# Kernel tuning notes

Hardware: AMD Instinct MI355X
Metric: run time of the kernel (lower is better)

## Reference

```python
import jax, jax.numpy as jnp
import numpy as np

T, B, D, H = 512, 64, 1024, 1024

def setup_inputs() -> dict:
    key = jax.random.key(0)
    k1, k2, k3 = jax.random.split(key, 3)
    x = jax.random.normal(k1, (T, B, D), dtype=jnp.float32)
    c0 = jnp.zeros((B, H), dtype=jnp.float32)
    h0 = jnp.zeros((B, H), dtype=jnp.float32)
    # fused gate weights, gate order (i, f, g, o) as in flax LSTMCell
    Wi = jax.random.normal(k2, (D, 4 * H), dtype=jnp.float32) / np.float32(np.sqrt(D))
    Wh = jax.random.normal(k3, (H, 4 * H), dtype=jnp.float32) / np.float32(np.sqrt(H))
    b = jnp.zeros((4 * H,), dtype=jnp.float32)
    return {"x": x, "c0": c0, "h0": h0, "Wi": Wi, "Wh": Wh, "b": b}

def reference(x, c0, h0, Wi, Wh, b):
    # scanned LSTM: per step z = x_t @ Wi + h @ Wh + b -> gates i,f,g,o
    def step(carry, xt):
        c, h = carry
        z = xt @ Wi + h @ Wh + b  # [B, 4H]
        i, f, g, o = jnp.split(z, 4, axis=-1)
        i = jax.nn.sigmoid(i)
        f = jax.nn.sigmoid(f)
        g = jnp.tanh(g)
        o = jax.nn.sigmoid(o)
        c_new = f * c + i * g
        h_new = o * jnp.tanh(c_new)
        return (c_new, h_new), h_new

    (cT, hT), ys = jax.lax.scan(step, (c0, h0), x)
    return ys, cT, hT
```

## Files before the change

### kernel.cpp

```cpp
#include <hip/hip_runtime.h>
#include <hip/hip_bf16.h>
#include <stdint.h>

typedef __attribute__((ext_vector_type(8))) short bf16x8;
typedef __attribute__((ext_vector_type(4))) float floatx4;

#define TT 512
#define BB 64
#define DD 1024
#define HH 1024
#define YS_ELEMS 33554432UL

#define OFF_A     0UL
#define OFF_XB    268435456UL
#define OFF_WIT   335544320UL
#define OFF_WHT   343932928UL
#define OFF_HBUF  352321536UL
#define OFF_FLAGS 352583680UL

#define NBLK 64
#define WPITCH 2064
#define LDSW_BYTES (64 * WPITCH)
#define LDSR_FLOATS (2 * 64 * 33)
#define SMEM_BYTES (LDSW_BYTES + LDSR_FLOATS * 4)

__device__ __forceinline__ unsigned short f2bf(float f) {
  union { float f; unsigned u; } v; v.f = f;
  unsigned r = (v.u + 0x7fffu + ((v.u >> 16) & 1u)) >> 16;
  return (unsigned short)r;
}
__device__ __forceinline__ float bf2f(unsigned short s) {
  union { unsigned u; float f; } v; v.u = ((unsigned)s) << 16;
  return v.f;
}
__device__ __forceinline__ float sigm(float x) { return 1.0f / (1.0f + __expf(-x)); }
__device__ __forceinline__ float tanh_fast(float x) { return 1.0f - 2.0f / (1.0f + __expf(2.0f * x)); }
__device__ __forceinline__ float ap_get(uint2 p, int r) {
  unsigned u = (r < 2) ? p.x : p.y;
  return bf2f((unsigned short)(u >> ((r & 1) * 16)));
}
__device__ __forceinline__ void gload_lds16(const void* g, void* l) {
  __builtin_amdgcn_global_load_lds((const __attribute__((address_space(1))) void*)g,
                                   (__attribute__((address_space(3))) void*)l, 16, 0, 0);
}
__device__ __forceinline__ bf16x8 ldg_b128_if(const void* p) {
  bf16x8 v;
  asm volatile("global_load_dwordx4 %0, %1, off sc0 sc1"
               : "=v"(v) : "v"(p) : "memory");
  return v;
}
__device__ __forceinline__ int ldg_b32_if(const void* p) {
  int v;
  asm volatile("global_load_dword %0, %1, off sc0 sc1\n\ts_waitcnt vmcnt(0)"
               : "=v"(v) : "v"(p) : "memory");
  return v;
}
__device__ __forceinline__ void stg_b64_if(void* p, uint2 v) {
  asm volatile("global_store_dwordx2 %0, %1, off sc0 sc1"
               :: "v"(p), "v"(v) : "memory");
}
__device__ __forceinline__ void stg_b32_if(void* p, int v) {
  asm volatile("global_store_dword %0, %1, off sc0 sc1"
               :: "v"(p), "v"(v) : "memory");
}

__global__ void convert_kernel(const float* __restrict__ x, const float* __restrict__ h0,
                               unsigned short* __restrict__ xb, unsigned short* __restrict__ hb0) {
  const long total4 = (33554432L + 65536L) / 4;
  long stride = (long)gridDim.x * blockDim.x;
  for (long i = (long)blockIdx.x * blockDim.x + threadIdx.x; i < total4; i += stride) {
    long base = i * 4;
    const float4* src;
    unsigned short* dst;
    if (base < 33554432L) { src = (const float4*)(x + base); dst = xb + base; }
    else { src = (const float4*)(h0 + (base - 33554432L)); dst = hb0 + (base - 33554432L); }
    float4 v = *src;
    uint2 p;
    p.x = (unsigned)f2bf(v.x) | ((unsigned)f2bf(v.y) << 16);
    p.y = (unsigned)f2bf(v.z) | ((unsigned)f2bf(v.w) << 16);
    *(uint2*)dst = p;
  }
}

__global__ void transpose_kernel(const float* __restrict__ W, unsigned short* __restrict__ WT) {
  __shared__ float tile[32][33];
  int n0 = blockIdx.x * 32, k0 = blockIdx.y * 32;
  int tx = threadIdx.x & 31, ty = threadIdx.x >> 5;
#pragma unroll
  for (int r = 0; r < 4; r++)
    tile[ty + r * 8][tx] = W[(size_t)(k0 + ty + r * 8) * 4096 + n0 + tx];
  __syncthreads();
#pragma unroll
  for (int r = 0; r < 4; r++)
    WT[(size_t)(n0 + ty + r * 8) * 1024 + k0 + tx] = f2bf(tile[tx][ty + r * 8]);
}

__global__ __launch_bounds__(256) void gemm1_kernel(const unsigned short* __restrict__ xb,
                                                    const unsigned short* __restrict__ wiT,
                                                    const float* __restrict__ bias,
                                                    unsigned short* __restrict__ Aws) {
  __shared__ unsigned short ldsA[128 * 32];
  __shared__ unsigned short ldsB[128 * 32];
  int id = blockIdx.x;
  int xcd = id & 7, seq = id >> 3;
  int n0 = (xcd * 4 + (seq & 3)) * 128;
  int m0 = (seq >> 2) * 128;
  int tid = threadIdx.x, w = tid >> 6, l = tid & 63;
  int wm = w & 1, wn = w >> 1;
  int c = l & 15, q = l >> 4;
  const floatx4 fz = {0.f, 0.f, 0.f, 0.f};
  floatx4 acc[4][4];
#pragma unroll
  for (int mi = 0; mi < 4; mi++)
#pragma unroll
    for (int ni = 0; ni < 4; ni++) acc[mi][ni] = fz;

  const char* gA = (const char*)xb + (size_t)(m0 + w * 32 + (l >> 2)) * 2048 + (l & 3) * 16;
  const char* gB = (const char*)wiT + (size_t)(n0 + w * 32 + (l >> 2)) * 2048 + (l & 3) * 16;
  char* lA = (char*)ldsA + (w * 32) * 64;
  char* lB = (char*)ldsB + (w * 32) * 64;

  for (int kt = 0; kt < 32; kt++) {
    gload_lds16(gA, lA);
    gload_lds16(gA + 16 * 2048, lA + 16 * 64);
    gload_lds16(gB, lB);
    gload_lds16(gB + 16 * 2048, lB + 16 * 64);
    gA += 64; gB += 64;
    __syncthreads();
    bf16x8 a[4], b[4];
#pragma unroll
    for (int mi = 0; mi < 4; mi++)
      a[mi] = *(const bf16x8*)((const char*)ldsA + (wm * 64 + mi * 16 + c) * 64 + q * 16);
#pragma unroll
    for (int ni = 0; ni < 4; ni++)
      b[ni] = *(const bf16x8*)((const char*)ldsB + (wn * 64 + ni * 16 + c) * 64 + q * 16);
#pragma unroll
    for (int mi = 0; mi < 4; mi++)
#pragma unroll
      for (int ni = 0; ni < 4; ni++)
        acc[mi][ni] = __builtin_amdgcn_mfma_f32_16x16x32_bf16(a[mi], b[ni], acc[mi][ni], 0, 0, 0);
    __syncthreads();
  }
#pragma unroll
  for (int mi = 0; mi < 4; mi++) {
#pragma unroll
    for (int ni = 0; ni < 4; ni++) {
      int n_g = n0 + wn * 64 + ni * 16 + c;
      float bn = bias[n_g];
      size_t mbase = (size_t)m0 + wm * 64 + mi * 16 + q * 4;
      floatx4 v = acc[mi][ni];
      uint2 p;
      p.x = (unsigned)f2bf(v.x + bn) | ((unsigned)f2bf(v.y + bn) << 16);
      p.y = (unsigned)f2bf(v.z + bn) | ((unsigned)f2bf(v.w + bn) << 16);
      *(uint2*)((char*)Aws + (((size_t)n_g << 15) + mbase) * 2) = p;
    }
  }
}

__global__ __launch_bounds__(256, 1) void lstm_kernel(const unsigned short* __restrict__ Aws,
                                                      const unsigned short* __restrict__ whT,
                                                      const float* __restrict__ c0,
                                                      unsigned short* __restrict__ hbuf,
                                                      float* __restrict__ out,
                                                      int* __restrict__ flags) {
  extern __shared__ char smem[];
  char* ldsW = smem;
  float* ldsR = (float*)(smem + LDSW_BYTES);
  int tid = threadIdx.x, wid = tid >> 6, l = tid & 63;
  int wi = wid & 1, wj = wid >> 1;
  int c = l & 15, q = l >> 4;
  int hbase = blockIdx.x * 16;

  for (int i = tid; i < 64 * 128; i += 256) {
    int ln = i >> 7, ch = i & 127;
    int n_g = (ln >> 4) * 1024 + hbase + (ln & 15);
    *(uint4*)(ldsW + ln * WPITCH + ch * 16) =
        *(const uint4*)((const char*)whT + (size_t)n_g * 2048 + ch * 16);
  }
  float cst[2][4];
  if (wj == 0) {
#pragma unroll
    for (int mi = 0; mi < 2; mi++)
#pragma unroll
      for (int r = 0; r < 4; r++)
        cst[mi][r] = c0[(wi * 32 + mi * 16 + q * 4 + r) * 1024 + hbase + c];
  }
  __syncthreads();

  for (int t = 0; t < 512; t++) {
    uint2 ap[2][4];
    if (wj == 0) {
#pragma unroll
      for (int mi = 0; mi < 2; mi++)
#pragma unroll
        for (int nj = 0; nj < 4; nj++) {
          size_t n_g = (size_t)nj * 1024 + hbase + c;
          ap[mi][nj] = *(const uint2*)((const char*)Aws +
                        ((n_g << 15) + (size_t)t * 64 + wi * 32 + mi * 16 + q * 4) * 2);
        }
    }

    if (wid == 0) {
      const char* fp_ = (const char*)(flags + l * 16);
      int probes = 0;
      for (;;) {
        int v = ldg_b32_if(fp_);
        if (__all(v >= t)) break;
        if (((++probes) & 2047) == 0)
          (void)__hip_atomic_load(&flags[l * 16], __ATOMIC_ACQUIRE, __HIP_MEMORY_SCOPE_AGENT);
      }
    }
    __syncthreads();
    asm volatile("s_waitcnt vmcnt(0)" ::: "memory");

    const char* hp = (const char*)hbuf + (size_t)(t & 1) * 131072;
    const char* ha0 = hp + (size_t)(wi * 32 + c) * 2048 + wj * 1024 + q * 16;
    const char* ha1 = ha0 + 16 * 2048;
    bf16x8 pf0[16], pf1[16];
#pragma unroll
    for (int kt = 0; kt < 16; kt++) {
      pf0[kt] = ldg_b128_if(ha0 + kt * 64);
      pf1[kt] = ldg_b128_if(ha1 + kt * 64);
    }
    const floatx4 fz = {0.f, 0.f, 0.f, 0.f};
    floatx4 acc[2][4];
#pragma unroll
    for (int mi = 0; mi < 2; mi++)
#pragma unroll
      for (int nj = 0; nj < 4; nj++) acc[mi][nj] = fz;

#pragma unroll
    for (int kt = 0; kt < 16; kt++) {
      bf16x8 b0 = *(const bf16x8*)(ldsW + (0 * 16 + c) * WPITCH + wj * 1024 + kt * 64 + q * 16);
      bf16x8 b1 = *(const bf16x8*)(ldsW + (1 * 16 + c) * WPITCH + wj * 1024 + kt * 64 + q * 16);
      bf16x8 b2 = *(const bf16x8*)(ldsW + (2 * 16 + c) * WPITCH + wj * 1024 + kt * 64 + q * 16);
      bf16x8 b3 = *(const bf16x8*)(ldsW + (3 * 16 + c) * WPITCH + wj * 1024 + kt * 64 + q * 16);
      asm volatile("s_waitcnt vmcnt(%0)" :: "n"(30 - 2 * kt) : "memory");
      __builtin_amdgcn_sched_barrier(0);
      acc[0][0] = __builtin_amdgcn_mfma_f32_16x16x32_bf16(pf0[kt], b0, acc[0][0], 0, 0, 0);
      acc[0][1] = __builtin_amdgcn_mfma_f32_16x16x32_bf16(pf0[kt], b1, acc[0][1], 0, 0, 0);
      acc[0][2] = __builtin_amdgcn_mfma_f32_16x16x32_bf16(pf0[kt], b2, acc[0][2], 0, 0, 0);
      acc[0][3] = __builtin_amdgcn_mfma_f32_16x16x32_bf16(pf0[kt], b3, acc[0][3], 0, 0, 0);
      acc[1][0] = __builtin_amdgcn_mfma_f32_16x16x32_bf16(pf1[kt], b0, acc[1][0], 0, 0, 0);
      acc[1][1] = __builtin_amdgcn_mfma_f32_16x16x32_bf16(pf1[kt], b1, acc[1][1], 0, 0, 0);
      acc[1][2] = __builtin_amdgcn_mfma_f32_16x16x32_bf16(pf1[kt], b2, acc[1][2], 0, 0, 0);
      acc[1][3] = __builtin_amdgcn_mfma_f32_16x16x32_bf16(pf1[kt], b3, acc[1][3], 0, 0, 0);
    }

    if (wj == 1) {
      float* p = ldsR + (size_t)(wi * 64 + l) * 33;
#pragma unroll
      for (int mi = 0; mi < 2; mi++)
#pragma unroll
        for (int nj = 0; nj < 4; nj++)
#pragma unroll
          for (int r = 0; r < 4; r++)
            p[mi * 16 + nj * 4 + r] = acc[mi][nj][r];
    }
    __syncthreads();

    float hreg[2][4], cnl[2][4];
    if (wj == 0) {
      const float* p = ldsR + (size_t)(wi * 64 + l) * 33;
#pragma unroll
      for (int mi = 0; mi < 2; mi++) {
#pragma unroll
        for (int r = 0; r < 4; r++) {
          float zi = acc[mi][0][r] + p[mi * 16 + 0 + r] + ap_get(ap[mi][0], r);
          float zf = acc[mi][1][r] + p[mi * 16 + 4 + r] + ap_get(ap[mi][1], r);
          float zg = acc[mi][2][r] + p[mi * 16 + 8 + r] + ap_get(ap[mi][2], r);
          float zo = acc[mi][3][r] + p[mi * 16 + 12 + r] + ap_get(ap[mi][3], r);
          float ig = sigm(zi), fg = sigm(zf);
          float tg = tanh_fast(zg), og = sigm(zo);
          float cn = fg * cst[mi][r] + ig * tg;
          cst[mi][r] = cn;
          cnl[mi][r] = cn;
          hreg[mi][r] = og * tanh_fast(cn);
        }
      }
      if (t < 511) {
        unsigned short* hn = hbuf + (size_t)(1 - (t & 1)) * 65536;
#pragma unroll
        for (int mi = 0; mi < 2; mi++)
#pragma unroll
          for (int r = 0; r < 4; r++) {
            unsigned hb = (unsigned)f2bf(hreg[mi][r]);
            unsigned p1 = (unsigned)__shfl_xor((int)hb, 1);
            unsigned lo = (hb & 0xffffu) | (p1 << 16);
            unsigned lo2 = (unsigned)__shfl_xor((int)lo, 2);
            if ((c & 3) == 0) {
              uint2 pk; pk.x = lo; pk.y = lo2;
              int row = wi * 32 + mi * 16 + q * 4 + r;
              stg_b64_if((char*)(hn + (size_t)row * 1024 + hbase + c), pk);
            }
          }
        asm volatile("s_waitcnt vmcnt(0)" ::: "memory");
      }
    }
    __syncthreads();
    if (t < 511 && tid == 0)
      stg_b32_if(flags + blockIdx.x * 16, t + 1);

    if (wj == 0) {
#pragma unroll
      for (int mi = 0; mi < 2; mi++)
#pragma unroll
        for (int r = 0; r < 4; r++) {
          int row = wi * 32 + mi * 16 + q * 4 + r;
          out[(size_t)t * 65536 + (size_t)row * 1024 + hbase + c] = hreg[mi][r];
          if (t == 511) {
            out[YS_ELEMS + (size_t)row * 1024 + hbase + c] = cnl[mi][r];
            out[YS_ELEMS + 65536 + (size_t)row * 1024 + hbase + c] = hreg[mi][r];
          }
        }
    }
  }
}

extern "C" void kernel_launch(void* const* d_in, const int* in_sizes, int n_in,
                              void* d_out, int out_size, void* d_ws, size_t ws_size,
                              hipStream_t stream) {
  (void)in_sizes; (void)n_in; (void)out_size; (void)ws_size;
  const float* x  = (const float*)d_in[0];
  const float* c0 = (const float*)d_in[1];
  const float* h0 = (const float*)d_in[2];
  const float* Wi = (const float*)d_in[3];
  const float* Wh = (const float*)d_in[4];
  const float* b  = (const float*)d_in[5];
  float* out = (float*)d_out;
  char* ws = (char*)d_ws;
  unsigned short* Aws  = (unsigned short*)(ws + OFF_A);
  unsigned short* xb   = (unsigned short*)(ws + OFF_XB);
  unsigned short* wiT  = (unsigned short*)(ws + OFF_WIT);
  unsigned short* whT  = (unsigned short*)(ws + OFF_WHT);
  unsigned short* hbuf = (unsigned short*)(ws + OFF_HBUF);
  int* flags = (int*)(ws + OFF_FLAGS);

  hipMemsetAsync(flags, 0, 4096, stream);
  convert_kernel<<<4096, 256, 0, stream>>>(x, h0, xb, hbuf);
  transpose_kernel<<<dim3(128, 32), 256, 0, stream>>>(Wi, wiT);
  transpose_kernel<<<dim3(128, 32), 256, 0, stream>>>(Wh, whT);
  gemm1_kernel<<<8192, 256, 0, stream>>>(xb, wiT, b, Aws);
  lstm_kernel<<<NBLK, 256, SMEM_BYTES, stream>>>(Aws, whT, c0, hbuf, out, flags);
}
```

Before: 4.772 ms.

## Replace flag-based inter-block barrier with canary-tagged 4-slot h buffer polling

Drops the per-step flag spin and block barrier that announced when h was ready. Each block instead polls the h slot it needs, reloading until no canary value is seen, and writes canaries into the slot two steps ahead so it can be reused. The hidden state now rotates through four slots (two reuse the xb workspace), and a new small kernel seeds the canaries before the recurrent kernel starts. This removes a separate flag round trip per step, but correctness now depends on a NaN-pattern canary never matching a real bf16 h value, and a whole-vector retry is issued whenever any lane sees a canary.

```diff
diff --git a/kernel.cpp b/kernel.cpp
--- a/kernel.cpp
+++ b/kernel.cpp
@@ -16,7 +16,6 @@
 #define OFF_WIT   335544320UL
 #define OFF_WHT   343932928UL
 #define OFF_HBUF  352321536UL
-#define OFF_FLAGS 352583680UL
 
 #define NBLK 64
 #define WPITCH 2064
@@ -24,6 +23,8 @@
 #define LDSR_FLOATS (2 * 64 * 33)
 #define SMEM_BYTES (LDSW_BYTES + LDSR_FLOATS * 4)
 
+#define CANARY 0x7FC07FC0u
+
 __device__ __forceinline__ unsigned short f2bf(float f) {
   union { float f; unsigned u; } v; v.f = f;
   unsigned r = (v.u + 0x7fffu + ((v.u >> 16) & 1u)) >> 16;
@@ -49,18 +50,8 @@
                : "=v"(v) : "v"(p) : "memory");
   return v;
 }
-__device__ __forceinline__ int ldg_b32_if(const void* p) {
-  int v;
-  asm volatile("global_load_dword %0, %1, off sc0 sc1\n\ts_waitcnt vmcnt(0)"
-               : "=v"(v) : "v"(p) : "memory");
-  return v;
-}
 __device__ __forceinline__ void stg_b64_if(void* p, uint2 v) {
   asm volatile("global_store_dwordx2 %0, %1, off sc0 sc1"
-               :: "v"(p), "v"(v) : "memory");
-}
-__device__ __forceinline__ void stg_b32_if(void* p, int v) {
-  asm volatile("global_store_dword %0, %1, off sc0 sc1"
                :: "v"(p), "v"(v) : "memory");
 }
 
@@ -82,6 +73,15 @@
   }
 }
 
+__global__ void canary_kernel(unsigned short* __restrict__ hb, unsigned short* __restrict__ hb2) {
+  int i = blockIdx.x * blockDim.x + threadIdx.x;
+  uint2 cv; cv.x = CANARY; cv.y = CANARY;
+  int slot = i >> 14;
+  int off = i & 16383;
+  unsigned short* base = (slot == 0) ? (hb + 65536) : (hb2 + (size_t)(slot - 1) * 65536);
+  *(uint2*)(base + (size_t)off * 4) = cv;
+}
+
 __global__ void transpose_kernel(const float* __restrict__ W, unsigned short* __restrict__ WT) {
   __shared__ float tile[32][33];
   int n0 = blockIdx.x * 32, k0 = blockIdx.y * 32;
@@ -161,8 +161,8 @@
                                                       const unsigned short* __restrict__ whT,
                                                       const float* __restrict__ c0,
                                                       unsigned short* __restrict__ hbuf,
-                                                      float* __restrict__ out,
-                                                      int* __restrict__ flags) {
+                                                      unsigned short* __restrict__ hbuf2,
+                                                      float* __restrict__ out) {
   extern __shared__ char smem[];
   char* ldsW = smem;
   float* ldsR = (float*)(smem + LDSW_BYTES);
@@ -188,6 +188,16 @@
   __syncthreads();
 
   for (int t = 0; t < 512; t++) {
+    int s_rd = t & 3;
+    const char* hp = (s_rd < 2) ? ((const char*)hbuf + (size_t)s_rd * 131072)
+                                : ((const char*)hbuf2 + (size_t)(s_rd - 2) * 131072);
+    int s_wr = (t + 1) & 3;
+    unsigned short* hn = (s_wr < 2) ? (hbuf + (size_t)s_wr * 65536)
+                                    : (hbuf2 + (size_t)(s_wr - 2) * 65536);
+    int s_fl = (t + 2) & 3;
+    unsigned short* hf = (s_fl < 2) ? (hbuf + (size_t)s_fl * 65536)
+                                    : (hbuf2 + (size_t)(s_fl - 2) * 65536);
+
     uint2 ap[2][4];
     if (wj == 0) {
 #pragma unroll
@@ -200,28 +210,34 @@
         }
     }
 
-    if (wid == 0) {
-      const char* fp_ = (const char*)(flags + l * 16);
-      int probes = 0;
-      for (;;) {
-        int v = ldg_b32_if(fp_);
-        if (__all(v >= t)) break;
-        if (((++probes) & 2047) == 0)
-          (void)__hip_atomic_load(&flags[l * 16], __ATOMIC_ACQUIRE, __HIP_MEMORY_SCOPE_AGENT);
-      }
-    }
-    __syncthreads();
-    asm volatile("s_waitcnt vmcnt(0)" ::: "memory");
-
-    const char* hp = (const char*)hbuf + (size_t)(t & 1) * 131072;
     const char* ha0 = hp + (size_t)(wi * 32 + c) * 2048 + wj * 1024 + q * 16;
     const char* ha1 = ha0 + 16 * 2048;
     bf16x8 pf0[16], pf1[16];
-#pragma unroll
-    for (int kt = 0; kt < 16; kt++) {
-      pf0[kt] = ldg_b128_if(ha0 + kt * 64);
-      pf1[kt] = ldg_b128_if(ha1 + kt * 64);
-    }
+    for (;;) {
+#pragma unroll
+      for (int kt = 0; kt < 16; kt++) {
+        pf0[kt] = ldg_b128_if(ha0 + kt * 64);
+        pf1[kt] = ldg_b128_if(ha1 + kt * 64);
+      }
+      asm volatile("s_waitcnt vmcnt(0)" ::: "memory");
+      __builtin_amdgcn_sched_barrier(0);
+      unsigned bad = 0u;
+#pragma unroll
+      for (int kt = 0; kt < 16; kt++) {
+        uint4 u0 = *(const uint4*)&pf0[kt];
+        uint4 u1 = *(const uint4*)&pf1[kt];
+        bad |= (unsigned)(u0.x == CANARY) | (unsigned)(u0.z == CANARY) |
+               (unsigned)(u1.x == CANARY) | (unsigned)(u1.z == CANARY);
+      }
+      if (__all(bad == 0u)) break;
+    }
+
+    if (t < 510) {
+      int row = tid >> 2, c4 = (tid & 3) * 4;
+      uint2 cv; cv.x = CANARY; cv.y = CANARY;
+      stg_b64_if((char*)(hf + (size_t)row * 1024 + hbase + c4), cv);
+    }
+
     const floatx4 fz = {0.f, 0.f, 0.f, 0.f};
     floatx4 acc[2][4];
 #pragma unroll
@@ -235,8 +251,6 @@
       bf16x8 b1 = *(const bf16x8*)(ldsW + (1 * 16 + c) * WPITCH + wj * 1024 + kt * 64 + q * 16);
       bf16x8 b2 = *(const bf16x8*)(ldsW + (2 * 16 + c) * WPITCH + wj * 1024 + kt * 64 + q * 16);
       bf16x8 b3 = *(const bf16x8*)(ldsW + (3 * 16 + c) * WPITCH + wj * 1024 + kt * 64 + q * 16);
-      asm volatile("s_waitcnt vmcnt(%0)" :: "n"(30 - 2 * kt) : "memory");
-      __builtin_amdgcn_sched_barrier(0);
       acc[0][0] = __builtin_amdgcn_mfma_f32_16x16x32_bf16(pf0[kt], b0, acc[0][0], 0, 0, 0);
       acc[0][1] = __builtin_amdgcn_mfma_f32_16x16x32_bf16(pf0[kt], b1, acc[0][1], 0, 0, 0);
       acc[0][2] = __builtin_amdgcn_mfma_f32_16x16x32_bf16(pf0[kt], b2, acc[0][2], 0, 0, 0);
@@ -279,7 +293,6 @@
         }
       }
       if (t < 511) {
-        unsigned short* hn = hbuf + (size_t)(1 - (t & 1)) * 65536;
 #pragma unroll
         for (int mi = 0; mi < 2; mi++)
 #pragma unroll
@@ -294,14 +307,7 @@
               stg_b64_if((char*)(hn + (size_t)row * 1024 + hbase + c), pk);
             }
           }
-        asm volatile("s_waitcnt vmcnt(0)" ::: "memory");
       }
-    }
-    __syncthreads();
-    if (t < 511 && tid == 0)
-      stg_b32_if(flags + blockIdx.x * 16, t + 1);
-
-    if (wj == 0) {
 #pragma unroll
       for (int mi = 0; mi < 2; mi++)
 #pragma unroll
@@ -314,6 +320,7 @@
           }
         }
     }
+    __syncthreads();
   }
 }
 
@@ -329,17 +336,17 @@
   const float* b  = (const float*)d_in[5];
   float* out = (float*)d_out;
   char* ws = (char*)d_ws;
-  unsigned short* Aws  = (unsigned short*)(ws + OFF_A);
-  unsigned short* xb   = (unsigned short*)(ws + OFF_XB);
-  unsigned short* wiT  = (unsigned short*)(ws + OFF_WIT);
-  unsigned short* whT  = (unsigned short*)(ws + OFF_WHT);
-  unsigned short* hbuf = (unsigned short*)(ws + OFF_HBUF);
-  int* flags = (int*)(ws + OFF_FLAGS);
-
-  hipMemsetAsync(flags, 0, 4096, stream);
+  unsigned short* Aws   = (unsigned short*)(ws + OFF_A);
+  unsigned short* xb    = (unsigned short*)(ws + OFF_XB);
+  unsigned short* wiT   = (unsigned short*)(ws + OFF_WIT);
+  unsigned short* whT   = (unsigned short*)(ws + OFF_WHT);
+  unsigned short* hbuf  = (unsigned short*)(ws + OFF_HBUF);
+  unsigned short* hbuf2 = (unsigned short*)(ws + OFF_XB);
+
   convert_kernel<<<4096, 256, 0, stream>>>(x, h0, xb, hbuf);
   transpose_kernel<<<dim3(128, 32), 256, 0, stream>>>(Wi, wiT);
   transpose_kernel<<<dim3(128, 32), 256, 0, stream>>>(Wh, whT);
   gemm1_kernel<<<8192, 256, 0, stream>>>(xb, wiT, b, Aws);
-  lstm_kernel<<<NBLK, 256, SMEM_BYTES, stream>>>(Aws, whT, c0, hbuf, out, flags);
-}
+  canary_kernel<<<192, 256, 0, stream>>>(hbuf, hbuf2);
+  lstm_kernel<<<NBLK, 256, SMEM_BYTES, stream>>>(Aws, whT, c0, hbuf, hbuf2, out);
+}
```

Result: slower. 5.573 ms (+16.8%).
